# Kernel optimization log

Measured on AMD Instinct MI355X. Metric: run time of the kernel, lower is better.

Reference implementation:

```python
import jax, jax.numpy as jnp
import numpy as np

HEAD_DIM = 64
N_HEADS = 16
D_MODEL = 2048
SEQ = 2048
BATCH = 1
LAYER_IDX = 12
LN_EPS = 1e-5


def setup_inputs() -> dict:
    key = jax.random.key(0)
    ks = jax.random.split(key, 8)
    s = 0.02
    return {
        "x": jax.random.normal(ks[0], (BATCH, SEQ, D_MODEL), dtype=jnp.float32),
        "W_qkv": jax.random.normal(ks[1], (3 * N_HEADS * 2 * HEAD_DIM, D_MODEL), dtype=jnp.float32) * s,
        "W_o": jax.random.normal(ks[2], (D_MODEL, D_MODEL), dtype=jnp.float32) * s,
        "lambda_q1": jax.random.normal(ks[3], (2 * HEAD_DIM,), dtype=jnp.float32) * 0.1,
        "lambda_k1": jax.random.normal(ks[4], (2 * HEAD_DIM,), dtype=jnp.float32) * 0.1,
        "lambda_q2": jax.random.normal(ks[5], (2 * HEAD_DIM,), dtype=jnp.float32) * 0.1,
        "lambda_k2": jax.random.normal(ks[6], (2 * HEAD_DIM,), dtype=jnp.float32) * 0.1,
        "gn_gamma": jnp.ones((N_HEADS, 2 * HEAD_DIM), dtype=jnp.float32),
        "gn_beta": jnp.zeros((N_HEADS, 2 * HEAD_DIM), dtype=jnp.float32),
    }


def _causal_sdpa(q, k, v, scale):
    # q,k: [B,H,S,d], v: [B,H,S,2d]
    S = q.shape[2]
    scores = jnp.einsum("bhqd,bhkd->bhqk", q, k) * scale
    causal = jnp.tril(jnp.ones((S, S), dtype=bool))
    scores = jnp.where(causal[None, None], scores, jnp.float32(-1e30))
    attn = jax.nn.softmax(scores, axis=-1)
    return jnp.einsum("bhqk,bhkd->bhqd", attn, v)


def reference(x, W_qkv, W_o, lambda_q1, lambda_k1, lambda_q2, lambda_k2, gn_gamma, gn_beta):
    B, S, D = x.shape
    lambda_init = 0.8 - 0.6 * jnp.exp(jnp.float32(-0.3 * LAYER_IDX))
    scale = HEAD_DIM ** -0.5

    qkv = x @ W_qkv.T  # [B,S,6*H*d]
    qkv = qkv.reshape(B, S, 3, N_HEADS, 2 * HEAD_DIM)
    q = jnp.transpose(qkv[:, :, 0], (0, 2, 1, 3))  # [B,H,S,2d]
    k = jnp.transpose(qkv[:, :, 1], (0, 2, 1, 3))
    v = jnp.transpose(qkv[:, :, 2], (0, 2, 1, 3))
    q1, q2 = q[..., :HEAD_DIM], q[..., HEAD_DIM:]
    k1, k2 = k[..., :HEAD_DIM], k[..., HEAD_DIM:]

    lam = jnp.exp(lambda_q1 * lambda_k1) - jnp.exp(lambda_q2 * lambda_k2) + lambda_init  # [2d]

    A1 = _causal_sdpa(q1, k1, v, scale)
    A2 = _causal_sdpa(q2, k2, v, scale)
    out = A1 - lam * A2  # broadcast over value channel [B,H,S,2d]

    # per-head LayerNorm over last dim
    mu = jnp.mean(out, axis=-1, keepdims=True)
    var = jnp.mean((out - mu) ** 2, axis=-1, keepdims=True)
    out = (out - mu) * jax.lax.rsqrt(var + LN_EPS)
    out = out * gn_gamma[None, :, None, :] + gn_beta[None, :, None, :]

    out = out * (1.0 - lambda_init)
    out = jnp.transpose(out, (0, 2, 1, 3)).reshape(B, S, D)
    return out @ W_o.T
```

## Files before the change

kernel.cpp:

```cpp
#include <hip/hip_runtime.h>

typedef short short8 __attribute__((ext_vector_type(8)));
typedef float f32x4 __attribute__((ext_vector_type(4)));
typedef unsigned short u16;
typedef u16 u16x8 __attribute__((ext_vector_type(8)));
typedef u16 u16x4 __attribute__((ext_vector_type(4)));

__device__ static inline u16 f2bf(float f) {
    union { float f; unsigned u; } v; v.f = f;
    unsigned r = v.u + 0x7fffu + ((v.u >> 16) & 1u);
    return (u16)(r >> 16);
}

__global__ __launch_bounds__(256) void cast_kernel(const float* __restrict__ in,
                                                   u16* __restrict__ out, int n) {
    int i = (blockIdx.x * 256 + threadIdx.x) * 4;
    if (i + 3 < n) {
        f32x4 v = *(const f32x4*)&in[i];
        u16x4 o;
        o[0] = f2bf(v[0]); o[1] = f2bf(v[1]); o[2] = f2bf(v[2]); o[3] = f2bf(v[3]);
        *(u16x4*)&out[i] = o;
    }
}

template <int BM, int BN, int MODE, int MINW>
__global__ __launch_bounds__(256, MINW) void gemm_bt(const u16* __restrict__ A,
                                                     const u16* __restrict__ B,
                                                     int M, int N, int K,
                                                     float* __restrict__ C,
                                                     u16* __restrict__ Qo,
                                                     u16* __restrict__ Ko,
                                                     u16* __restrict__ Vo) {
    constexpr int APT = BM * 4 / 256;
    constexpr int BPT = BN * 4 / 256;
    constexpr int MT = BM / 32, NT = BN / 32;
    __shared__ u16 As[BM * 32];
    __shared__ u16 Bs[BN * 32];
    const int tid  = threadIdx.x;
    const int lane = tid & 63, wave = tid >> 6;
    const int quad = lane >> 4, l15 = lane & 15;
    const int wm = wave >> 1, wn = wave & 1;
    const int m0 = blockIdx.y * BM;
    const int n0 = blockIdx.x * BN;

    f32x4 acc[MT][NT] = {};

    const u16* aga[APT];
    const u16* bga[BPT];
#pragma unroll
    for (int i = 0; i < APT; i++) {
        int s = tid + i * 256, r = s >> 2;
        int kg = (s & 3) ^ ((r >> 1) & 3);
        aga[i] = &A[(size_t)(m0 + r) * K + kg * 8];
    }
#pragma unroll
    for (int i = 0; i < BPT; i++) {
        int s = tid + i * 256, r = s >> 2;
        int kg = (s & 3) ^ ((r >> 1) & 3);
        bga[i] = &B[(size_t)(n0 + r) * K + kg * 8];
    }

    u16x8 ast[APT], bst[BPT];
#pragma unroll
    for (int i = 0; i < APT; i++) ast[i] = *(const u16x8*)aga[i];
#pragma unroll
    for (int i = 0; i < BPT; i++) bst[i] = *(const u16x8*)bga[i];

    for (int k0 = 0; k0 < K; k0 += 32) {
        if (k0) __syncthreads();
#pragma unroll
        for (int i = 0; i < APT; i++) *(u16x8*)&As[(tid + i * 256) * 8] = ast[i];
#pragma unroll
        for (int i = 0; i < BPT; i++) *(u16x8*)&Bs[(tid + i * 256) * 8] = bst[i];
        __syncthreads();
        if (k0 + 32 < K) {
#pragma unroll
            for (int i = 0; i < APT; i++) ast[i] = *(const u16x8*)(aga[i] + k0 + 32);
#pragma unroll
            for (int i = 0; i < BPT; i++) bst[i] = *(const u16x8*)(bga[i] + k0 + 32);
        }

        short8 af[MT], bf[NT];
#pragma unroll
        for (int mt = 0; mt < MT; mt++) {
            int row = wm * (BM / 2) + mt * 16 + l15;
            int slot = row * 4 + (quad ^ ((row >> 1) & 3));
            af[mt] = *(const short8*)&As[slot * 8];
        }
#pragma unroll
        for (int nt = 0; nt < NT; nt++) {
            int row = wn * (BN / 2) + nt * 16 + l15;
            int slot = row * 4 + (quad ^ ((row >> 1) & 3));
            bf[nt] = *(const short8*)&Bs[slot * 8];
        }
#pragma unroll
        for (int mt = 0; mt < MT; mt++)
#pragma unroll
            for (int nt = 0; nt < NT; nt++)
                acc[mt][nt] = __builtin_amdgcn_mfma_f32_16x16x32_bf16(af[mt], bf[nt], acc[mt][nt], 0, 0, 0);
    }

    if (MODE == 0) {
#pragma unroll
        for (int mt = 0; mt < MT; mt++)
#pragma unroll
            for (int nt = 0; nt < NT; nt++)
#pragma unroll
                for (int r = 0; r < 4; r++) {
                    int row = m0 + wm * (BM / 2) + mt * 16 + quad * 4 + r;
                    int col = n0 + wn * (BN / 2) + nt * 16 + l15;
                    C[(size_t)row * N + col] = acc[mt][nt][r];
                }
    } else {
        const int comp = n0 >> 11, h = (n0 >> 7) & 15;
        u16* dst = (comp == 0) ? Qo : ((comp == 1) ? Ko : Vo);
        const float sc = (comp == 0) ? 0.18033688f : 1.0f;
#pragma unroll
        for (int mt = 0; mt < MT; mt++)
#pragma unroll
            for (int nt = 0; nt < NT; nt++)
#pragma unroll
                for (int r = 0; r < 4; r++) {
                    int row = m0 + wm * (BM / 2) + mt * 16 + quad * 4 + r;
                    int d = wn * (BN / 2) + nt * 16 + l15;
                    dst[((h * 2048) + row) * 128 + d] = f2bf(acc[mt][nt][r] * sc);
                }
    }
}

__global__ __launch_bounds__(256) void transpose_v(const u16* __restrict__ vb,
                                                   u16* __restrict__ vT) {
    __shared__ u16 T[64 * 136];
    const int s0 = blockIdx.x * 64, h = blockIdx.y;
    const int tid = threadIdx.x;
#pragma unroll
    for (int i = 0; i < 4; i++) {
        int c = tid + i * 256;
        int s = c >> 4, dch = c & 15;
        *(u16x8*)&T[s * 136 + dch * 8] =
            *(const u16x8*)&vb[((h * 2048) + s0 + s) * 128 + dch * 8];
    }
    __syncthreads();
#pragma unroll
    for (int i = 0; i < 4; i++) {
        int c = tid + i * 256;
        int d = c >> 3, sch = c & 7;
        u16x8 o;
#pragma unroll
        for (int j = 0; j < 8; j++) o[j] = T[(sch * 8 + j) * 136 + d];
        *(u16x8*)&vT[((h * 128) + d) * 2048 + s0 + sch * 8] = o;
    }
}

__global__ __launch_bounds__(256, 4) void attn_kernel(const u16* __restrict__ qb,
                                                      const u16* __restrict__ kb,
                                                      const u16* __restrict__ vT,
                                                      float* __restrict__ ob) {
    const int bid = blockIdx.x;
    const int h = bid & 15;
    const int comp = (bid >> 4) & 1;
    const int j = bid >> 5;
    const int qt = (j < 16) ? (2 * j + 1) : (62 - 2 * j);
    const int tid = threadIdx.x, lane = tid & 63, wave = tid >> 6;
    const int quad = lane >> 4, l15 = lane & 15;

    __shared__ u16 Ks[64 * 64];
    __shared__ u16 VsT[128 * 64];
    __shared__ u16 Ps[4][16 * 72];

    const u16* kb_h = &kb[(size_t)h * 2048 * 128 + comp * 64];
    const u16* vT_h = &vT[(size_t)h * 128 * 2048];

    const int c1 = tid, c2 = tid + 256;
    const int k1key = c1 >> 3, k1dc = ((c1 & 7) ^ k1key) & 7;
    const int k2key = c2 >> 3, k2dc = ((c2 & 7) ^ k2key) & 7;
    const u16* kaddr1 = &kb_h[k1key * 128 + k1dc * 8];
    const u16* kaddr2 = &kb_h[k2key * 128 + k2dc * 8];
    const u16* vaddr[4];
#pragma unroll
    for (int i = 0; i < 4; i++) {
        int c = tid + i * 256;
        int dim = c >> 3, kc = ((c & 7) ^ dim) & 7;
        vaddr[i] = &vT_h[dim * 2048 + kc * 8];
    }

    const int qrow = qt * 64 + wave * 16 + l15;
    short8 aq[2];
#pragma unroll
    for (int ks = 0; ks < 2; ks++)
        aq[ks] = *(const short8*)&qb[((h * 2048) + qrow) * 128 + comp * 64 + ks * 32 + quad * 8];

    float l_acc[4] = {0.f, 0.f, 0.f, 0.f};
    f32x4 o[8] = {};

    u16x8 kst0, kst1, vst[4];
    kst0 = *(const u16x8*)(kaddr1);
    kst1 = *(const u16x8*)(kaddr2);
#pragma unroll
    for (int i = 0; i < 4; i++) vst[i] = *(const u16x8*)(vaddr[i]);

    for (int kt = 0; kt <= qt; kt++) {
        *(u16x8*)&Ks[c1 * 8] = kst0;
        *(u16x8*)&Ks[c2 * 8] = kst1;
#pragma unroll
        for (int i = 0; i < 4; i++) *(u16x8*)&VsT[(tid + i * 256) * 8] = vst[i];
        __syncthreads();

        if (kt < qt) {
            const int nkt = kt + 1;
            kst0 = *(const u16x8*)(kaddr1 + nkt * 8192);
            kst1 = *(const u16x8*)(kaddr2 + nkt * 8192);
#pragma unroll
            for (int i = 0; i < 4; i++) vst[i] = *(const u16x8*)(vaddr[i] + nkt * 64);
        }

        f32x4 s[4];
#pragma unroll
        for (int kn = 0; kn < 4; kn++) {
            f32x4 a = {};
#pragma unroll
            for (int ks = 0; ks < 2; ks++) {
                int key = kn * 16 + l15;
                int dc = ks * 4 + quad;
                short8 b = *(const short8*)&Ks[(key * 8 + ((dc ^ key) & 7)) * 8];
                a = __builtin_amdgcn_mfma_f32_16x16x32_bf16(aq[ks], b, a, 0, 0, 0);
            }
            s[kn] = a;
        }
        if (kt == qt) {
#pragma unroll
            for (int kn = 0; kn < 4; kn++)
#pragma unroll
                for (int r = 0; r < 4; r++) {
                    int ql = wave * 16 + quad * 4 + r, kl = kn * 16 + l15;
                    if (kl > ql) s[kn][r] = -1e30f;
                }
        }

        u16* pw = &Ps[wave][0];
#pragma unroll
        for (int kn = 0; kn < 4; kn++)
#pragma unroll
            for (int r = 0; r < 4; r++) {
                float p = exp2f(s[kn][r]);
                l_acc[r] += p;
                pw[(quad * 4 + r) * 72 + kn * 16 + l15] = f2bf(p);
            }
        asm volatile("s_waitcnt lgkmcnt(0)\n" ::: "memory");

#pragma unroll
        for (int ks2 = 0; ks2 < 2; ks2++) {
            short8 pa = *(const short8*)&pw[l15 * 72 + ks2 * 32 + quad * 8];
#pragma unroll
            for (int nt = 0; nt < 8; nt++) {
                int dim = nt * 16 + l15;
                int kc = ks2 * 4 + quad;
                short8 bv = *(const short8*)&VsT[(dim * 8 + ((kc ^ dim) & 7)) * 8];
                o[nt] = __builtin_amdgcn_mfma_f32_16x16x32_bf16(pa, bv, o[nt], 0, 0, 0);
            }
        }
        __syncthreads();
    }

#pragma unroll
    for (int off = 1; off < 16; off <<= 1)
#pragma unroll
        for (int r = 0; r < 4; r++) l_acc[r] += __shfl_xor(l_acc[r], off);
    float rl[4];
#pragma unroll
    for (int r = 0; r < 4; r++) rl[r] = 1.f / l_acc[r];

    const int srow = qt * 64 + wave * 16 + quad * 4;
#pragma unroll
    for (int nt = 0; nt < 8; nt++)
#pragma unroll
        for (int r = 0; r < 4; r++) {
            float v = o[nt][r] * rl[r];
            ob[(((comp * 16 + h) * 2048) + srow + r) * 128 + nt * 16 + l15] = v;
        }
}

__global__ __launch_bounds__(256) void combine_kernel(const float* __restrict__ ob,
                                                      const float* __restrict__ lq1,
                                                      const float* __restrict__ lk1,
                                                      const float* __restrict__ lq2,
                                                      const float* __restrict__ lk2,
                                                      const float* __restrict__ gamma,
                                                      const float* __restrict__ beta,
                                                      u16* __restrict__ attn) {
    const int tid = threadIdx.x, wave = tid >> 6, lane = tid & 63;
    const int row = blockIdx.x * 4 + wave;
    const int s = row >> 4, h = row & 15;
    const float lambda_init = 0.8f - 0.6f * __expf(-3.6f);
    const int d0 = lane * 2;
    float vals[2];
#pragma unroll
    for (int j = 0; j < 2; j++) {
        int d = d0 + j;
        float a1 = ob[((h)*2048 + s) * 128 + d];
        float a2 = ob[((16 + h) * 2048 + s) * 128 + d];
        float lam = __expf(lq1[d] * lk1[d]) - __expf(lq2[d] * lk2[d]) + lambda_init;
        vals[j] = a1 - lam * a2;
    }
    float sum = vals[0] + vals[1];
    float sq = vals[0] * vals[0] + vals[1] * vals[1];
#pragma unroll
    for (int off = 1; off < 64; off <<= 1) {
        sum += __shfl_xor(sum, off);
        sq += __shfl_xor(sq, off);
    }
    float mu = sum * (1.f / 128.f);
    float var = sq * (1.f / 128.f) - mu * mu;
    float rinv = rsqrtf(var + 1e-5f);
    float osc = 1.f - lambda_init;
#pragma unroll
    for (int j = 0; j < 2; j++) {
        int d = d0 + j;
        float g = gamma[h * 128 + d], b = beta[h * 128 + d];
        float v = ((vals[j] - mu) * rinv * g + b) * osc;
        attn[s * 2048 + h * 128 + d] = f2bf(v);
    }
}

extern "C" void kernel_launch(void* const* d_in, const int* in_sizes, int n_in,
                              void* d_out, int out_size, void* d_ws, size_t ws_size,
                              hipStream_t stream) {
    (void)in_sizes; (void)n_in; (void)out_size; (void)ws_size;
    const float* x    = (const float*)d_in[0];
    const float* Wqkv = (const float*)d_in[1];
    const float* Wo   = (const float*)d_in[2];
    const float* lq1  = (const float*)d_in[3];
    const float* lk1  = (const float*)d_in[4];
    const float* lq2  = (const float*)d_in[5];
    const float* lk2  = (const float*)d_in[6];
    const float* gam  = (const float*)d_in[7];
    const float* bet  = (const float*)d_in[8];
    float* out = (float*)d_out;

    char* ws = (char*)d_ws;
    u16*   xb    = (u16*)(ws);
    u16*   wqkvb = (u16*)(ws + (size_t)(8 << 20));
    float* ob    = (float*)(ws + (size_t)(8 << 20));
    u16*   wob   = (u16*)(ws + (size_t)(40 << 20));
    u16*   qb    = (u16*)(ws + (size_t)(48 << 20));
    u16*   kb    = (u16*)(ws + (size_t)(56 << 20));
    u16*   vb    = (u16*)(ws + (size_t)(64 << 20));
    u16*   vT    = (u16*)(ws + (size_t)(72 << 20));
    u16*   attn  = (u16*)(ws);

    cast_kernel<<<(2048 * 2048) / 1024, 256, 0, stream>>>(x, xb, 2048 * 2048);
    cast_kernel<<<(6144 * 2048) / 1024, 256, 0, stream>>>(Wqkv, wqkvb, 6144 * 2048);
    cast_kernel<<<(2048 * 2048) / 1024, 256, 0, stream>>>(Wo, wob, 2048 * 2048);
    gemm_bt<128, 128, 1, 3><<<dim3(48, 16), 256, 0, stream>>>(
        xb, wqkvb, 2048, 6144, 2048, nullptr, qb, kb, vb);
    transpose_v<<<dim3(32, 16), 256, 0, stream>>>(vb, vT);
    attn_kernel<<<1024, 256, 0, stream>>>(qb, kb, vT, ob);
    combine_kernel<<<8192, 256, 0, stream>>>(ob, lq1, lk1, lq2, lk2, gam, bet, attn);
    gemm_bt<128, 64, 0, 2><<<dim3(32, 16), 256, 0, stream>>>(
        attn, wob, 2048, 2048, 2048, out, nullptr, nullptr, nullptr);
}
```

Before: 298.6 us.

## Use 128-row query tiles and keep P in registers via transposed score MFMA

The attention kernel now handles 128 query rows per block (two 16-row subtiles per wave), so each K/V tile loaded into shared memory serves twice as many queries and the grid halves to 512 blocks. Scores are computed transposed (K as the A operand), so each lane holds probabilities already in the layout needed for the PV MFMA, and they are fed directly as a half-filled (zero-padded) 16x16x32 operand. This removes the per-wave shared-memory staging of P along with its waitcnt. The cost is twice as many PV MFMAs for the same work, higher register pressure (occupancy hint lowered from 4 to 2), and fewer blocks to balance the causal workload.

```diff
diff --git a/kernel.cpp b/kernel.cpp
--- a/kernel.cpp
+++ b/kernel.cpp
@@ -152,7 +152,7 @@
     }
 }
 
-__global__ __launch_bounds__(256, 4) void attn_kernel(const u16* __restrict__ qb,
+__global__ __launch_bounds__(256, 2) void attn_kernel(const u16* __restrict__ qb,
                                                       const u16* __restrict__ kb,
                                                       const u16* __restrict__ vT,
                                                       float* __restrict__ ob) {
@@ -160,13 +160,14 @@
     const int h = bid & 15;
     const int comp = (bid >> 4) & 1;
     const int j = bid >> 5;
-    const int qt = (j < 16) ? (2 * j + 1) : (62 - 2 * j);
+    const int J = (j < 8) ? (2 * j + 1) : (30 - 2 * j);
+    const int nkt = 2 * J + 2;
+    const int q0 = J * 128;
     const int tid = threadIdx.x, lane = tid & 63, wave = tid >> 6;
     const int quad = lane >> 4, l15 = lane & 15;
 
     __shared__ u16 Ks[64 * 64];
     __shared__ u16 VsT[128 * 64];
-    __shared__ u16 Ps[4][16 * 72];
 
     const u16* kb_h = &kb[(size_t)h * 2048 * 128 + comp * 64];
     const u16* vT_h = &vT[(size_t)h * 128 * 2048];
@@ -184,14 +185,18 @@
         vaddr[i] = &vT_h[dim * 2048 + kc * 8];
     }
 
-    const int qrow = qt * 64 + wave * 16 + l15;
-    short8 aq[2];
-#pragma unroll
-    for (int ks = 0; ks < 2; ks++)
-        aq[ks] = *(const short8*)&qb[((h * 2048) + qrow) * 128 + comp * 64 + ks * 32 + quad * 8];
-
-    float l_acc[4] = {0.f, 0.f, 0.f, 0.f};
-    f32x4 o[8] = {};
+    short8 aq[2][2];
+#pragma unroll
+    for (int qs = 0; qs < 2; qs++)
+#pragma unroll
+        for (int ks = 0; ks < 2; ks++) {
+            int qrow = q0 + wave * 32 + qs * 16 + l15;
+            aq[qs][ks] = *(const short8*)
+                &qb[((h * 2048) + qrow) * 128 + comp * 64 + ks * 32 + quad * 8];
+        }
+
+    float l_acc[2] = {0.f, 0.f};
+    f32x4 acc[8][2] = {};
 
     u16x8 kst0, kst1, vst[4];
     kst0 = *(const u16x8*)(kaddr1);
@@ -199,85 +204,86 @@
 #pragma unroll
     for (int i = 0; i < 4; i++) vst[i] = *(const u16x8*)(vaddr[i]);
 
-    for (int kt = 0; kt <= qt; kt++) {
+    for (int kt = 0; kt < nkt; kt++) {
         *(u16x8*)&Ks[c1 * 8] = kst0;
         *(u16x8*)&Ks[c2 * 8] = kst1;
 #pragma unroll
         for (int i = 0; i < 4; i++) *(u16x8*)&VsT[(tid + i * 256) * 8] = vst[i];
         __syncthreads();
 
-        if (kt < qt) {
-            const int nkt = kt + 1;
-            kst0 = *(const u16x8*)(kaddr1 + nkt * 8192);
-            kst1 = *(const u16x8*)(kaddr2 + nkt * 8192);
-#pragma unroll
-            for (int i = 0; i < 4; i++) vst[i] = *(const u16x8*)(vaddr[i] + nkt * 64);
-        }
-
-        f32x4 s[4];
-#pragma unroll
-        for (int kn = 0; kn < 4; kn++) {
-            f32x4 a = {};
-#pragma unroll
-            for (int ks = 0; ks < 2; ks++) {
-                int key = kn * 16 + l15;
-                int dc = ks * 4 + quad;
-                short8 b = *(const short8*)&Ks[(key * 8 + ((dc ^ key) & 7)) * 8];
-                a = __builtin_amdgcn_mfma_f32_16x16x32_bf16(aq[ks], b, a, 0, 0, 0);
+        if (kt + 1 < nkt) {
+            const int nkt1 = kt + 1;
+            kst0 = *(const u16x8*)(kaddr1 + nkt1 * 8192);
+            kst1 = *(const u16x8*)(kaddr2 + nkt1 * 8192);
+#pragma unroll
+            for (int i = 0; i < 4; i++) vst[i] = *(const u16x8*)(vaddr[i] + nkt1 * 64);
+        }
+
+        short8 b8[2][4];
+#pragma unroll
+        for (int qs = 0; qs < 2; qs++) {
+#pragma unroll
+            for (int kn = 0; kn < 4; kn++) {
+                f32x4 st = {};
+#pragma unroll
+                for (int ks = 0; ks < 2; ks++) {
+                    int key = kn * 16 + l15;
+                    int dc = ks * 4 + quad;
+                    short8 kf = *(const short8*)&Ks[(key * 8 + ((dc ^ key) & 7)) * 8];
+                    st = __builtin_amdgcn_mfma_f32_16x16x32_bf16(kf, aq[qs][ks], st, 0, 0, 0);
+                }
+                if (kt >= nkt - 2) {
+                    int q = q0 + wave * 32 + qs * 16 + l15;
+#pragma unroll
+                    for (int r = 0; r < 4; r++) {
+                        int key = kt * 64 + kn * 16 + quad * 4 + r;
+                        if (key > q) st[r] = -1e30f;
+                    }
+                }
+                float p0 = exp2f(st[0]), p1 = exp2f(st[1]);
+                float p2 = exp2f(st[2]), p3 = exp2f(st[3]);
+                l_acc[qs] += (p0 + p1) + (p2 + p3);
+                b8[qs][kn] = short8{(short)f2bf(p0), (short)f2bf(p1),
+                                    (short)f2bf(p2), (short)f2bf(p3), 0, 0, 0, 0};
             }
-            s[kn] = a;
-        }
-        if (kt == qt) {
-#pragma unroll
-            for (int kn = 0; kn < 4; kn++)
-#pragma unroll
-                for (int r = 0; r < 4; r++) {
-                    int ql = wave * 16 + quad * 4 + r, kl = kn * 16 + l15;
-                    if (kl > ql) s[kn][r] = -1e30f;
-                }
-        }
-
-        u16* pw = &Ps[wave][0];
-#pragma unroll
-        for (int kn = 0; kn < 4; kn++)
-#pragma unroll
-            for (int r = 0; r < 4; r++) {
-                float p = exp2f(s[kn][r]);
-                l_acc[r] += p;
-                pw[(quad * 4 + r) * 72 + kn * 16 + l15] = f2bf(p);
+        }
+
+#pragma unroll
+        for (int nt = 0; nt < 8; nt++) {
+            int dim = nt * 16 + l15;
+#pragma unroll
+            for (int kn = 0; kn < 4; kn++) {
+                int g = kn * 2 + (quad >> 1);
+                int sc = (g ^ dim) & 7;
+                u16x4 a4 = *(const u16x4*)&VsT[dim * 64 + sc * 8 + (quad & 1) * 4];
+                short8 a8 = short8{(short)a4[0], (short)a4[1], (short)a4[2], (short)a4[3],
+                                   0, 0, 0, 0};
+                acc[nt][0] = __builtin_amdgcn_mfma_f32_16x16x32_bf16(a8, b8[0][kn], acc[nt][0], 0, 0, 0);
+                acc[nt][1] = __builtin_amdgcn_mfma_f32_16x16x32_bf16(a8, b8[1][kn], acc[nt][1], 0, 0, 0);
             }
-        asm volatile("s_waitcnt lgkmcnt(0)\n" ::: "memory");
-
-#pragma unroll
-        for (int ks2 = 0; ks2 < 2; ks2++) {
-            short8 pa = *(const short8*)&pw[l15 * 72 + ks2 * 32 + quad * 8];
-#pragma unroll
-            for (int nt = 0; nt < 8; nt++) {
-                int dim = nt * 16 + l15;
-                int kc = ks2 * 4 + quad;
-                short8 bv = *(const short8*)&VsT[(dim * 8 + ((kc ^ dim) & 7)) * 8];
-                o[nt] = __builtin_amdgcn_mfma_f32_16x16x32_bf16(pa, bv, o[nt], 0, 0, 0);
-            }
         }
         __syncthreads();
     }
 
 #pragma unroll
-    for (int off = 1; off < 16; off <<= 1)
-#pragma unroll
-        for (int r = 0; r < 4; r++) l_acc[r] += __shfl_xor(l_acc[r], off);
-    float rl[4];
-#pragma unroll
-    for (int r = 0; r < 4; r++) rl[r] = 1.f / l_acc[r];
-
-    const int srow = qt * 64 + wave * 16 + quad * 4;
-#pragma unroll
-    for (int nt = 0; nt < 8; nt++)
-#pragma unroll
-        for (int r = 0; r < 4; r++) {
-            float v = o[nt][r] * rl[r];
-            ob[(((comp * 16 + h) * 2048) + srow + r) * 128 + nt * 16 + l15] = v;
-        }
+    for (int qs = 0; qs < 2; qs++) {
+        l_acc[qs] += __shfl_xor(l_acc[qs], 16);
+        l_acc[qs] += __shfl_xor(l_acc[qs], 32);
+    }
+    float rl[2] = {1.f / l_acc[0], 1.f / l_acc[1]};
+
+#pragma unroll
+    for (int qs = 0; qs < 2; qs++) {
+        int s = q0 + wave * 32 + qs * 16 + l15;
+        float* orow = &ob[((size_t)(comp * 16 + h) * 2048 + s) * 128 + quad * 4];
+#pragma unroll
+        for (int nt = 0; nt < 8; nt++) {
+            f32x4 v;
+#pragma unroll
+            for (int r = 0; r < 4; r++) v[r] = acc[nt][qs][r] * rl[qs];
+            *(f32x4*)&orow[nt * 16] = v;
+        }
+    }
 }
 
 __global__ __launch_bounds__(256) void combine_kernel(const float* __restrict__ ob,
@@ -354,7 +360,7 @@
     gemm_bt<128, 128, 1, 3><<<dim3(48, 16), 256, 0, stream>>>(
         xb, wqkvb, 2048, 6144, 2048, nullptr, qb, kb, vb);
     transpose_v<<<dim3(32, 16), 256, 0, stream>>>(vb, vT);
-    attn_kernel<<<1024, 256, 0, stream>>>(qb, kb, vT, ob);
+    attn_kernel<<<512, 256, 0, stream>>>(qb, kb, vT, ob);
     combine_kernel<<<8192, 256, 0, stream>>>(ob, lq1, lk1, lq2, lk2, gam, bet, attn);
     gemm_bt<128, 64, 0, 2><<<dim3(32, 16), 256, 0, stream>>>(
         attn, wob, 2048, 2048, 2048, out, nullptr, nullptr, nullptr);
```

After: 294.2 us. No clear change (-1.5%).
